# Performance work log

Measured on AMD Instinct MI355X. Metric: run time of the kernel, lower is better.

The kernel has to match this reference:

```python
import jax, jax.numpy as jnp
import numpy as np

N_WIRES = 12
DIM = 2 ** N_WIRES  # 4096 = seq_len * embed_dim

_H = np.array([[1, 1], [1, -1]], dtype=np.complex64) / np.sqrt(2.0)
_CNOT = np.array([[1, 0, 0, 0],
                  [0, 1, 0, 0],
                  [0, 0, 0, 1],
                  [0, 0, 1, 0]], dtype=np.complex64)
_SWAP = np.array([[1, 0, 0, 0],
                  [0, 0, 1, 0],
                  [0, 1, 0, 0],
                  [0, 0, 0, 1]], dtype=np.complex64)

def _cp_mat(theta):
    m = np.eye(4, dtype=np.complex64)
    m[3, 3] = np.exp(1j * theta)
    return m

def _apply_gate(state, U, wires):
    # state: (B,) + (2,)*N_WIRES ; U: (2^k, 2^k) acting on `wires` (wire 0 = MSB = axis 1)
    k = len(wires)
    src = [w + 1 for w in wires]
    dst = list(range(1, k + 1))
    st = jnp.moveaxis(state, src, dst)
    sh = st.shape
    st = st.reshape(sh[0], 2 ** k, -1)
    st = jnp.einsum('ij,bjr->bir', jnp.asarray(U), st)
    return jnp.moveaxis(st.reshape(sh), dst, src)

def _cnot_ring(state):
    for i in range(N_WIRES):
        state = _apply_gate(state, _CNOT, [i, (i + 1) % N_WIRES])
    return state

def _qft(state):
    for m in range(N_WIRES - 1, 0, -1):
        state = _apply_gate(state, _H, [m])
        for i in range(m):
            state = _apply_gate(state, _cp_mat(np.pi / 2 ** (m - i)), [i, m])
    for i in range(N_WIRES // 2):
        state = _apply_gate(state, _SWAP, [i, N_WIRES - i - 1])
    return state

def _full_unitary(state, U):
    # dense 2^n x 2^n unitary over the whole register: psi' = U @ psi
    b = state.shape[0]
    flat = state.reshape(b, DIM)
    return jnp.einsum('ij,bj->bi', U, flat).reshape(state.shape)

def setup_inputs() -> dict:
    key = jax.random.key(0)
    k1, k2, k3 = jax.random.split(key, 3)
    x = jax.random.normal(k1, (128, 64, 64), dtype=jnp.float32)
    scale = DIM ** -0.5  # keep applied matrices roughly norm-preserving
    U_re = jax.random.normal(k2, (4, DIM, DIM), dtype=jnp.float32) * scale
    U_im = jax.random.normal(k3, (4, DIM, DIM), dtype=jnp.float32) * scale
    return {"x": x, "U_re": U_re, "U_im": U_im}

def reference(x, U_re, U_im):
    B, S, E = x.shape
    flat = x.reshape(B, S * E)
    pad = DIM - flat.shape[1]
    if pad > 0:
        flat = jnp.pad(flat, ((0, 0), (0, pad)))
    # StateEncoder: L2-normalize and lift to complex statevector
    norm = jnp.sqrt(jnp.sum(flat * flat, axis=-1, keepdims=True))
    psi = (flat / norm).astype(jnp.complex64)
    state = psi.reshape((B,) + (2,) * N_WIRES)
    U = (U_re + 1j * U_im).astype(jnp.complex64)
    # vqc(0)
    state = _full_unitary(state, U[0])
    state = _cnot_ring(state)
    state = _full_unitary(state, U[1])
    # qft
    state = _qft(state)
    # vqc(1)
    state = _full_unitary(state, U[2])
    state = _cnot_ring(state)
    state = _full_unitary(state, U[3])
    out = jnp.abs(state.reshape(B, DIM))
    return out.reshape(B, S, E)
```

## Files before the change

### kernel.cpp

```cpp
#include <hip/hip_runtime.h>
#include <hip/hip_bf16.h>
#include <math.h>

#define N_WIRES 12
#define DIM     4096
#define BATCH   128
#define BD      (BATCH*DIM)
#define BM      128
#define BN      32
#define BK      64
#define KS      4
#define KCHUNK  (DIM / KS)

typedef __attribute__((ext_vector_type(4))) float f32x4;
typedef __attribute__((ext_vector_type(4))) unsigned int u32x4;
typedef __bf16 bf16x8 __attribute__((ext_vector_type(8)));
typedef __attribute__((ext_vector_type(8))) unsigned short us8;

__device__ __forceinline__ f32x4 mfma16(bf16x8 a, bf16x8 b, f32x4 c){
  return __builtin_amdgcn_mfma_f32_16x16x32_bf16(a, b, c, 0, 0, 0);
}

__device__ __forceinline__ void gload16(const void* g, void* l){
  __builtin_amdgcn_global_load_lds(
    (const __attribute__((address_space(1))) unsigned int*)g,
    (__attribute__((address_space(3))) unsigned int*)l, 16, 0, 0);
}


__global__ void k_normalize(const float* __restrict__ x, __hip_bfloat16* __restrict__ dst){
  const int b = blockIdx.x, t = threadIdx.x;
  const float4* xr = reinterpret_cast<const float4*>(x + (size_t)b * DIM);
  float4 v[4];
  float ss = 0.f;
  #pragma unroll
  for (int r = 0; r < 4; ++r){
    v[r] = xr[t*4 + r];
    ss += v[r].x*v[r].x + v[r].y*v[r].y + v[r].z*v[r].z + v[r].w*v[r].w;
  }
  #pragma unroll
  for (int off = 32; off > 0; off >>= 1) ss += __shfl_down(ss, off);
  __shared__ float sred[4];
  if ((t & 63) == 0) sred[t >> 6] = ss;
  __syncthreads();
  const float inv = 1.f / sqrtf(sred[0] + sred[1] + sred[2] + sred[3]);
  #pragma unroll
  for (int h = 0; h < 2; ++h){
    union { __bf16 e[8]; us8 s; } pk;
    const float* vv = reinterpret_cast<const float*>(&v[h*2]);
    #pragma unroll
    for (int j = 0; j < 8; ++j) pk.e[j] = (__bf16)(vv[j] * inv);
    const int j0 = t*16 + h*8;
    const int sc = ((j0 >> 3) & 7) ^ (b & 7);
    *reinterpret_cast<us8*>(dst + (size_t)b*DIM + (j0 & ~63) + sc*8) = pk.s;
  }
}

template<bool CIN>
__global__ __launch_bounds__(256, 2) void k_gemm(
    const float* __restrict__ Ure, const float* __restrict__ Uim,
    const __hip_bfloat16* __restrict__ X, float* __restrict__ P)
{
  constexpr int NCC = CIN ? 2 : 1;
  __shared__ __bf16 Xs[NCC*BM*BK];
  __shared__ __bf16 Us[2*BN*BK];
  const int t = threadIdx.x;
  const int lane = t & 63, wid = t >> 6;
  const int n0 = blockIdx.x * BN;
  const int kb = blockIdx.y * KCHUNK;

  const f32x4 z4 = {0.f,0.f,0.f,0.f};
  f32x4 acc[2][2][2];
  #pragma unroll
  for (int mi = 0; mi < 2; ++mi)
    #pragma unroll
    for (int ni = 0; ni < 2; ++ni){ acc[mi][ni][0] = z4; acc[mi][ni][1] = z4; }

  for (int kk = 0; kk < KCHUNK; kk += BK){
    __syncthreads();
    #pragma unroll
    for (int r = 0; r < NCC*4; ++r){
      const int idx = r*256 + t;
      const int c   = idx >> 10;
      const int ci  = idx & 1023;
      const int row = ci >> 3, sc = ci & 7;
      const __hip_bfloat16* src = X + (size_t)c*BD + (size_t)row*DIM + (kb + kk) + sc*8;
      gload16(src, &Xs[idx*8]);
    }
    float4 uv[4];
    #pragma unroll
    for (int r = 0; r < 4; ++r){
      const int idx = r*256 + t;
      const int c = idx >> 9, ci = idx & 511;
      const int row = ci >> 4, q = ci & 15;
      const float* us = c ? Uim : Ure;
      uv[r] = *reinterpret_cast<const float4*>(us + (size_t)(n0 + row)*DIM + (kb + kk) + q*4);
    }
    #pragma unroll
    for (int r = 0; r < 4; ++r){
      const int idx = r*256 + t;
      const int c = idx >> 9, ci = idx & 511;
      const int row = ci >> 4, q = ci & 15;
      union { __bf16 h[4]; unsigned long long u; } pk;
      pk.h[0]=(__bf16)uv[r].x; pk.h[1]=(__bf16)uv[r].y;
      pk.h[2]=(__bf16)uv[r].z; pk.h[3]=(__bf16)uv[r].w;
      const int e = (((q >> 1) ^ (row & 7)) << 3) | ((q & 1) << 2);
      *reinterpret_cast<unsigned long long*>(&Us[c*BN*BK + row*BK + e]) = pk.u;
    }
    __syncthreads();

    #pragma unroll
    for (int ks = 0; ks < 2; ++ks){
      const int lc = ks*4 + (lane >> 4);
      bf16x8 ar[2], ai[2], br[2], bi[2];
      #pragma unroll
      for (int mi = 0; mi < 2; ++mi){
        const int row = wid*32 + mi*16 + (lane & 15);
        const int off = row*BK + ((lc ^ (row & 7)) << 3);
        ar[mi] = *reinterpret_cast<const bf16x8*>(&Xs[off]);
        if (CIN) ai[mi] = *reinterpret_cast<const bf16x8*>(&Xs[BM*BK + off]);
      }
      #pragma unroll
      for (int ni = 0; ni < 2; ++ni){
        const int row = ni*16 + (lane & 15);
        const int off = row*BK + ((lc ^ (row & 7)) << 3);
        br[ni] = *reinterpret_cast<const bf16x8*>(&Us[off]);
        bi[ni] = *reinterpret_cast<const bf16x8*>(&Us[BN*BK + off]);
      }
      #pragma unroll
      for (int mi = 0; mi < 2; ++mi){
        bf16x8 an = ar[mi];
        if (CIN){
          const u32x4 negu = __builtin_bit_cast(u32x4, ai[mi]) ^ 0x80008000u;
          an = __builtin_bit_cast(bf16x8, negu);
        }
        #pragma unroll
        for (int ni = 0; ni < 2; ++ni){
          acc[mi][ni][0] = mfma16(ar[mi], br[ni], acc[mi][ni][0]);
          acc[mi][ni][1] = mfma16(ar[mi], bi[ni], acc[mi][ni][1]);
          if (CIN){
            acc[mi][ni][0] = mfma16(an,     bi[ni], acc[mi][ni][0]);
            acc[mi][ni][1] = mfma16(ai[mi], br[ni], acc[mi][ni][1]);
          }
        }
      }
    }
  }
  float* pre = P + (size_t)(blockIdx.y*2 + 0)*BD;
  float* pim = P + (size_t)(blockIdx.y*2 + 1)*BD;
  #pragma unroll
  for (int mi = 0; mi < 2; ++mi)
    #pragma unroll
    for (int ni = 0; ni < 2; ++ni){
      const int col = n0 + ni*16 + (lane & 15);
      const int m0 = wid*32 + mi*16 + (lane >> 4)*4;
      #pragma unroll
      for (int j = 0; j < 4; ++j){
        pre[(size_t)(m0+j)*DIM + col] = acc[mi][ni][0][j];
        pim[(size_t)(m0+j)*DIM + col] = acc[mi][ni][1][j];
      }
    }
}

__device__ __forceinline__ int cnot_dst(int x){
  #pragma unroll
  for (int i = 0; i < 12; ++i){
    const int cb = 11 - i;
    const int tb = 11 - ((i + 1) % 12);
    x ^= ((x >> cb) & 1) << tb;
  }
  return x;
}

__global__ void k_perm(const float* __restrict__ P, __hip_bfloat16* __restrict__ dst){
  const int idx = blockIdx.x * 256 + threadIdx.x;
  const int b = idx >> 12;
  const int m = idx & (DIM - 1);
  float re = 0.f, im = 0.f;
  #pragma unroll
  for (int s = 0; s < KS; ++s){
    re += P[(size_t)(s*2+0)*BD + (size_t)b*DIM + m];
    im += P[(size_t)(s*2+1)*BD + (size_t)b*DIM + m];
  }
  const int k = cnot_dst(m);
  const int e = (k & ~63) | (((((k >> 3) & 7) ^ (b & 7)) << 3)) | (k & 7);
  dst[(size_t)b*DIM + e] = __float2bfloat16(re);
  dst[(size_t)BD + (size_t)b*DIM + e] = __float2bfloat16(im);
}

__global__ void k_abs(const float* __restrict__ P, float* __restrict__ dst){
  const int idx = blockIdx.x * 256 + threadIdx.x;
  const int b = idx >> 12;
  const int m = idx & (DIM - 1);
  float re = 0.f, im = 0.f;
  #pragma unroll
  for (int s = 0; s < KS; ++s){
    re += P[(size_t)(s*2+0)*BD + (size_t)b*DIM + m];
    im += P[(size_t)(s*2+1)*BD + (size_t)b*DIM + m];
  }
  dst[idx] = sqrtf(re*re + im*im);
}

__global__ void k_qft(const float* __restrict__ P, __hip_bfloat16* __restrict__ out){
  __shared__ float sre[DIM];
  __shared__ float sim[DIM];
  const int b = blockIdx.x, t = threadIdx.x;
  for (int i = t; i < DIM; i += 512){
    float re = 0.f, im = 0.f;
    #pragma unroll
    for (int s = 0; s < KS; ++s){
      re += P[(size_t)(s*2+0)*BD + (size_t)b*DIM + i];
      im += P[(size_t)(s*2+1)*BD + (size_t)b*DIM + i];
    }
    sre[i] = re; sim[i] = im;
  }
  __syncthreads();
  const float rs2 = 0.70710678118654752440f;
  for (int m = 11; m >= 1; --m){
    const int p = 11 - m;
    const int mask = 1 << p;
    for (int q = t; q < 2048; q += 512){
      const int i0 = ((q & ~(mask-1)) << 1) | (q & (mask-1));
      const int i1 = i0 | mask;
      const float r0 = sre[i0], s0 = sim[i0], r1 = sre[i1], s1 = sim[i1];
      sre[i0] = (r0 + r1) * rs2; sim[i0] = (s0 + s1) * rs2;
      sre[i1] = (r0 - r1) * rs2; sim[i1] = (s0 - s1) * rs2;
    }
    __syncthreads();
    for (int q = t; q < 2048; q += 512){
      const int i1 = (((q & ~(mask-1)) << 1) | (q & (mask-1))) | mask;
      int u = i1 >> (p + 1);
      float phi = 0.f, w = 1.57079632679489662f;
      while (u){ if (u & 1) phi += w; w *= 0.5f; u >>= 1; }
      float cc, ss;
      __sincosf(phi, &ss, &cc);
      const float r = sre[i1], q2 = sim[i1];
      sre[i1] = r*cc - q2*ss;
      sim[i1] = r*ss + q2*cc;
    }
    __syncthreads();
  }
  for (int i = t; i < DIM; i += 512){
    const int rsrc = (int)(__brev((unsigned)i) >> 20);
    const int e = (i & ~63) | (((((i >> 3) & 7) ^ (b & 7)) << 3)) | (i & 7);
    out[(size_t)b*DIM + e] = __float2bfloat16(sre[rsrc]);
    out[(size_t)BD + (size_t)b*DIM + e] = __float2bfloat16(sim[rsrc]);
  }
}

extern "C" void kernel_launch(void* const* d_in, const int* in_sizes, int n_in,
                              void* d_out, int out_size, void* d_ws, size_t ws_size,
                              hipStream_t stream){
  const float* x   = (const float*)d_in[0];
  const float* Ure = (const float*)d_in[1];
  const float* Uim = (const float*)d_in[2];
  float* out = (float*)d_out;

  float* P = (float*)d_ws;
  __hip_bfloat16* B0 = (__hip_bfloat16*)(P + (size_t)KS*2*BD);
  __hip_bfloat16* B1 = B0 + (size_t)2*BD;
  const size_t UST = (size_t)DIM*DIM;
  const dim3 gg(DIM/BN, KS);

  k_normalize<<<BATCH, 256, 0, stream>>>(x, B0);
  k_gemm<false><<<gg, 256, 0, stream>>>(Ure, Uim, B0, P);
  k_perm<<<BD/256, 256, 0, stream>>>(P, B1);
  k_gemm<true><<<gg, 256, 0, stream>>>(Ure + UST, Uim + UST, B1, P);
  k_qft<<<BATCH, 512, 0, stream>>>(P, B0);
  k_gemm<true><<<gg, 256, 0, stream>>>(Ure + 2*UST, Uim + 2*UST, B0, P);
  k_perm<<<BD/256, 256, 0, stream>>>(P, B1);
  k_gemm<true><<<gg, 256, 0, stream>>>(Ure + 3*UST, Uim + 3*UST, B1, P);
  k_abs<<<BD/256, 256, 0, stream>>>(P, out);
}
```

Measured before the change: 209.8 us.

## Double-buffer GEMM staging and store split-K partials in bf16

The GEMM main loop now double-buffers the X and U shared-memory tiles. It issues global loads for the next K tile, including register prefetch of the fp32 U rows, before computing the current one, and uses explicit vmcnt waits and barriers. Split-K partial sums are written as bf16 instead of fp32, which halves the partial-buffer write and read traffic. The reduction kernels (perm, abs, qft load) are vectorized to handle 8 elements per thread. This adds extra rounding of the partials to bf16 and doubles LDS use, which may reduce occupancy.

```diff
diff --git a/kernel.cpp b/kernel.cpp
--- a/kernel.cpp
+++ b/kernel.cpp
@@ -27,6 +27,13 @@
     (__attribute__((address_space(3))) unsigned int*)l, 16, 0, 0);
 }
 
+__device__ __forceinline__ float bf2f(unsigned short u){
+  union { unsigned int i; float f; } cv; cv.i = ((unsigned int)u) << 16; return cv.f;
+}
+
+__device__ __forceinline__ int swz(int j, int b){
+  return (j & ~63) | (((((j >> 3) & 7) ^ (b & 7))) << 3) | (j & 7);
+}
 
 __global__ void k_normalize(const float* __restrict__ x, __hip_bfloat16* __restrict__ dst){
   const int b = blockIdx.x, t = threadIdx.x;
@@ -51,19 +58,19 @@
     #pragma unroll
     for (int j = 0; j < 8; ++j) pk.e[j] = (__bf16)(vv[j] * inv);
     const int j0 = t*16 + h*8;
-    const int sc = ((j0 >> 3) & 7) ^ (b & 7);
-    *reinterpret_cast<us8*>(dst + (size_t)b*DIM + (j0 & ~63) + sc*8) = pk.s;
+    *reinterpret_cast<us8*>(dst + (size_t)b*DIM + swz(j0, b)) = pk.s;
   }
 }
 
 template<bool CIN>
 __global__ __launch_bounds__(256, 2) void k_gemm(
     const float* __restrict__ Ure, const float* __restrict__ Uim,
-    const __hip_bfloat16* __restrict__ X, float* __restrict__ P)
+    const __hip_bfloat16* __restrict__ X, __hip_bfloat16* __restrict__ P)
 {
   constexpr int NCC = CIN ? 2 : 1;
-  __shared__ __bf16 Xs[NCC*BM*BK];
-  __shared__ __bf16 Us[2*BN*BK];
+  constexpr int NT  = KCHUNK / BK;
+  __shared__ __bf16 Xs[2][NCC*BM*BK];
+  __shared__ __bf16 Us[2][2*BN*BK];
   const int t = threadIdx.x;
   const int lane = t & 63, wid = t >> 6;
   const int n0 = blockIdx.x * BN;
@@ -76,26 +83,26 @@
     #pragma unroll
     for (int ni = 0; ni < 2; ++ni){ acc[mi][ni][0] = z4; acc[mi][ni][1] = z4; }
 
-  for (int kk = 0; kk < KCHUNK; kk += BK){
-    __syncthreads();
+  auto stageX = [&](int kk, int bf){
     #pragma unroll
     for (int r = 0; r < NCC*4; ++r){
       const int idx = r*256 + t;
-      const int c   = idx >> 10;
-      const int ci  = idx & 1023;
+      const int c = idx >> 10, ci = idx & 1023;
       const int row = ci >> 3, sc = ci & 7;
-      const __hip_bfloat16* src = X + (size_t)c*BD + (size_t)row*DIM + (kb + kk) + sc*8;
-      gload16(src, &Xs[idx*8]);
-    }
-    float4 uv[4];
+      gload16(X + (size_t)c*BD + (size_t)row*DIM + kb + kk + sc*8, &Xs[bf][idx*8]);
+    }
+  };
+  auto loadU = [&](int kk, float4 (&uv)[4]){
     #pragma unroll
     for (int r = 0; r < 4; ++r){
       const int idx = r*256 + t;
       const int c = idx >> 9, ci = idx & 511;
       const int row = ci >> 4, q = ci & 15;
       const float* us = c ? Uim : Ure;
-      uv[r] = *reinterpret_cast<const float4*>(us + (size_t)(n0 + row)*DIM + (kb + kk) + q*4);
-    }
+      uv[r] = *reinterpret_cast<const float4*>(us + (size_t)(n0 + row)*DIM + kb + kk + q*4);
+    }
+  };
+  auto writeU = [&](const float4 (&uv)[4], int bf){
     #pragma unroll
     for (int r = 0; r < 4; ++r){
       const int idx = r*256 + t;
@@ -105,10 +112,10 @@
       pk.h[0]=(__bf16)uv[r].x; pk.h[1]=(__bf16)uv[r].y;
       pk.h[2]=(__bf16)uv[r].z; pk.h[3]=(__bf16)uv[r].w;
       const int e = (((q >> 1) ^ (row & 7)) << 3) | ((q & 1) << 2);
-      *reinterpret_cast<unsigned long long*>(&Us[c*BN*BK + row*BK + e]) = pk.u;
-    }
-    __syncthreads();
-
+      *reinterpret_cast<unsigned long long*>(&Us[bf][c*BN*BK + row*BK + e]) = pk.u;
+    }
+  };
+  auto compute = [&](int bf){
     #pragma unroll
     for (int ks = 0; ks < 2; ++ks){
       const int lc = ks*4 + (lane >> 4);
@@ -117,15 +124,15 @@
       for (int mi = 0; mi < 2; ++mi){
         const int row = wid*32 + mi*16 + (lane & 15);
         const int off = row*BK + ((lc ^ (row & 7)) << 3);
-        ar[mi] = *reinterpret_cast<const bf16x8*>(&Xs[off]);
-        if (CIN) ai[mi] = *reinterpret_cast<const bf16x8*>(&Xs[BM*BK + off]);
+        ar[mi] = *reinterpret_cast<const bf16x8*>(&Xs[bf][off]);
+        if (CIN) ai[mi] = *reinterpret_cast<const bf16x8*>(&Xs[bf][BM*BK + off]);
       }
       #pragma unroll
       for (int ni = 0; ni < 2; ++ni){
         const int row = ni*16 + (lane & 15);
         const int off = row*BK + ((lc ^ (row & 7)) << 3);
-        br[ni] = *reinterpret_cast<const bf16x8*>(&Us[off]);
-        bi[ni] = *reinterpret_cast<const bf16x8*>(&Us[BN*BK + off]);
+        br[ni] = *reinterpret_cast<const bf16x8*>(&Us[bf][off]);
+        bi[ni] = *reinterpret_cast<const bf16x8*>(&Us[bf][BN*BK + off]);
       }
       #pragma unroll
       for (int mi = 0; mi < 2; ++mi){
@@ -145,9 +152,40 @@
         }
       }
     }
-  }
-  float* pre = P + (size_t)(blockIdx.y*2 + 0)*BD;
-  float* pim = P + (size_t)(blockIdx.y*2 + 1)*BD;
+  };
+
+  float4 uvA[4], uvB[4];
+  stageX(0, 0);
+  loadU(0, uvA);
+
+#define GSTEP(TT, UVC, UVN)                                                    \
+  {                                                                            \
+    const int cur = (TT) & 1;                                                  \
+    if ((TT) + 1 < NT){                                                        \
+      stageX(((TT)+1)*BK, cur ^ 1);                                            \
+      loadU(((TT)+1)*BK, UVN);                                                 \
+      if constexpr (CIN) asm volatile("s_waitcnt vmcnt(12)" ::: "memory");     \
+      else               asm volatile("s_waitcnt vmcnt(8)"  ::: "memory");     \
+    } else {                                                                   \
+      asm volatile("s_waitcnt vmcnt(0)" ::: "memory");                         \
+    }                                                                          \
+    __builtin_amdgcn_sched_barrier(0);                                         \
+    writeU(UVC, cur);                                                          \
+    asm volatile("s_waitcnt lgkmcnt(0)" ::: "memory");                         \
+    __builtin_amdgcn_s_barrier();                                              \
+    compute(cur);                                                              \
+    __builtin_amdgcn_sched_barrier(0);                                         \
+    __builtin_amdgcn_s_barrier();                                              \
+  }
+
+  for (int t2 = 0; t2 < NT; t2 += 2){
+    GSTEP(t2,     uvA, uvB);
+    GSTEP(t2 + 1, uvB, uvA);
+  }
+#undef GSTEP
+
+  __hip_bfloat16* pre = P + (size_t)(blockIdx.y*2 + 0)*BD;
+  __hip_bfloat16* pim = P + (size_t)(blockIdx.y*2 + 1)*BD;
   #pragma unroll
   for (int mi = 0; mi < 2; ++mi)
     #pragma unroll
@@ -156,8 +194,8 @@
       const int m0 = wid*32 + mi*16 + (lane >> 4)*4;
       #pragma unroll
       for (int j = 0; j < 4; ++j){
-        pre[(size_t)(m0+j)*DIM + col] = acc[mi][ni][0][j];
-        pim[(size_t)(m0+j)*DIM + col] = acc[mi][ni][1][j];
+        pre[(size_t)(m0+j)*DIM + col] = __float2bfloat16(acc[mi][ni][0][j]);
+        pim[(size_t)(m0+j)*DIM + col] = __float2bfloat16(acc[mi][ni][1][j]);
       }
     }
 }
@@ -172,47 +210,74 @@
   return x;
 }
 
-__global__ void k_perm(const float* __restrict__ P, __hip_bfloat16* __restrict__ dst){
-  const int idx = blockIdx.x * 256 + threadIdx.x;
-  const int b = idx >> 12;
-  const int m = idx & (DIM - 1);
-  float re = 0.f, im = 0.f;
+__global__ void k_perm(const __hip_bfloat16* __restrict__ P, __hip_bfloat16* __restrict__ dst){
+  const int g = blockIdx.x * 256 + threadIdx.x;
+  const int b = g >> 9;
+  const int m0 = (g & 511) * 8;
+  float re[8], im[8];
+  #pragma unroll
+  for (int j = 0; j < 8; ++j){ re[j] = 0.f; im[j] = 0.f; }
   #pragma unroll
   for (int s = 0; s < KS; ++s){
-    re += P[(size_t)(s*2+0)*BD + (size_t)b*DIM + m];
-    im += P[(size_t)(s*2+1)*BD + (size_t)b*DIM + m];
-  }
-  const int k = cnot_dst(m);
-  const int e = (k & ~63) | (((((k >> 3) & 7) ^ (b & 7)) << 3)) | (k & 7);
-  dst[(size_t)b*DIM + e] = __float2bfloat16(re);
-  dst[(size_t)BD + (size_t)b*DIM + e] = __float2bfloat16(im);
-}
-
-__global__ void k_abs(const float* __restrict__ P, float* __restrict__ dst){
-  const int idx = blockIdx.x * 256 + threadIdx.x;
-  const int b = idx >> 12;
-  const int m = idx & (DIM - 1);
-  float re = 0.f, im = 0.f;
+    const us8 vr = *reinterpret_cast<const us8*>(P + (size_t)(s*2+0)*BD + (size_t)b*DIM + m0);
+    const us8 vi = *reinterpret_cast<const us8*>(P + (size_t)(s*2+1)*BD + (size_t)b*DIM + m0);
+    #pragma unroll
+    for (int j = 0; j < 8; ++j){
+      re[j] += bf2f(vr[j]);
+      im[j] += bf2f(vi[j]);
+    }
+  }
+  #pragma unroll
+  for (int j = 0; j < 8; ++j){
+    const int e = swz(cnot_dst(m0 + j), b);
+    dst[(size_t)b*DIM + e] = __float2bfloat16(re[j]);
+    dst[(size_t)BD + (size_t)b*DIM + e] = __float2bfloat16(im[j]);
+  }
+}
+
+__global__ void k_abs(const __hip_bfloat16* __restrict__ P, float* __restrict__ dst){
+  const int g = blockIdx.x * 256 + threadIdx.x;
+  const int b = g >> 9;
+  const int m0 = (g & 511) * 8;
+  float re[8], im[8];
+  #pragma unroll
+  for (int j = 0; j < 8; ++j){ re[j] = 0.f; im[j] = 0.f; }
   #pragma unroll
   for (int s = 0; s < KS; ++s){
-    re += P[(size_t)(s*2+0)*BD + (size_t)b*DIM + m];
-    im += P[(size_t)(s*2+1)*BD + (size_t)b*DIM + m];
-  }
-  dst[idx] = sqrtf(re*re + im*im);
-}
-
-__global__ void k_qft(const float* __restrict__ P, __hip_bfloat16* __restrict__ out){
+    const us8 vr = *reinterpret_cast<const us8*>(P + (size_t)(s*2+0)*BD + (size_t)b*DIM + m0);
+    const us8 vi = *reinterpret_cast<const us8*>(P + (size_t)(s*2+1)*BD + (size_t)b*DIM + m0);
+    #pragma unroll
+    for (int j = 0; j < 8; ++j){
+      re[j] += bf2f(vr[j]);
+      im[j] += bf2f(vi[j]);
+    }
+  }
+  #pragma unroll
+  for (int j = 0; j < 8; ++j)
+    dst[(size_t)b*DIM + m0 + j] = sqrtf(re[j]*re[j] + im[j]*im[j]);
+}
+
+__global__ void k_qft(const __hip_bfloat16* __restrict__ P, __hip_bfloat16* __restrict__ out){
   __shared__ float sre[DIM];
   __shared__ float sim[DIM];
   const int b = blockIdx.x, t = threadIdx.x;
-  for (int i = t; i < DIM; i += 512){
-    float re = 0.f, im = 0.f;
+  {
+    const int m0 = t * 8;
+    float re[8], im[8];
+    #pragma unroll
+    for (int j = 0; j < 8; ++j){ re[j] = 0.f; im[j] = 0.f; }
     #pragma unroll
     for (int s = 0; s < KS; ++s){
-      re += P[(size_t)(s*2+0)*BD + (size_t)b*DIM + i];
-      im += P[(size_t)(s*2+1)*BD + (size_t)b*DIM + i];
-    }
-    sre[i] = re; sim[i] = im;
+      const us8 vr = *reinterpret_cast<const us8*>(P + (size_t)(s*2+0)*BD + (size_t)b*DIM + m0);
+      const us8 vi = *reinterpret_cast<const us8*>(P + (size_t)(s*2+1)*BD + (size_t)b*DIM + m0);
+      #pragma unroll
+      for (int j = 0; j < 8; ++j){
+        re[j] += bf2f(vr[j]);
+        im[j] += bf2f(vi[j]);
+      }
+    }
+    #pragma unroll
+    for (int j = 0; j < 8; ++j){ sre[m0+j] = re[j]; sim[m0+j] = im[j]; }
   }
   __syncthreads();
   const float rs2 = 0.70710678118654752440f;
@@ -242,7 +307,7 @@
   }
   for (int i = t; i < DIM; i += 512){
     const int rsrc = (int)(__brev((unsigned)i) >> 20);
-    const int e = (i & ~63) | (((((i >> 3) & 7) ^ (b & 7)) << 3)) | (i & 7);
+    const int e = swz(i, b);
     out[(size_t)b*DIM + e] = __float2bfloat16(sre[rsrc]);
     out[(size_t)BD + (size_t)b*DIM + e] = __float2bfloat16(sim[rsrc]);
   }
@@ -256,19 +321,19 @@
   const float* Uim = (const float*)d_in[2];
   float* out = (float*)d_out;
 
-  float* P = (float*)d_ws;
-  __hip_bfloat16* B0 = (__hip_bfloat16*)(P + (size_t)KS*2*BD);
+  __hip_bfloat16* P  = (__hip_bfloat16*)d_ws;
+  __hip_bfloat16* B0 = P + (size_t)KS*2*BD;
   __hip_bfloat16* B1 = B0 + (size_t)2*BD;
   const size_t UST = (size_t)DIM*DIM;
   const dim3 gg(DIM/BN, KS);
 
   k_normalize<<<BATCH, 256, 0, stream>>>(x, B0);
   k_gemm<false><<<gg, 256, 0, stream>>>(Ure, Uim, B0, P);
-  k_perm<<<BD/256, 256, 0, stream>>>(P, B1);
+  k_perm<<<BD/2048, 256, 0, stream>>>(P, B1);
   k_gemm<true><<<gg, 256, 0, stream>>>(Ure + UST, Uim + UST, B1, P);
   k_qft<<<BATCH, 512, 0, stream>>>(P, B0);
   k_gemm<true><<<gg, 256, 0, stream>>>(Ure + 2*UST, Uim + 2*UST, B0, P);
-  k_perm<<<BD/256, 256, 0, stream>>>(P, B1);
+  k_perm<<<BD/2048, 256, 0, stream>>>(P, B1);
   k_gemm<true><<<gg, 256, 0, stream>>>(Ure + 3*UST, Uim + 3*UST, B1, P);
-  k_abs<<<BD/256, 256, 0, stream>>>(P, out);
-}
+  k_abs<<<BD/2048, 256, 0, stream>>>(P, out);
+}
```

New measurement: 215.7 us. 2.8% more time.
